# Kernel optimization log

Hardware: AMD Instinct MI355X
Metric: run time of the kernel (lower is better)

The kernel has to match this reference:

```python
import jax, jax.numpy as jnp
import numpy as np

N = 50000   # nodes
E = 600000  # directed edges
B = 128     # graphs
IN = 128
H = 128
K = 30      # sort-pool k
C_OUT = 32
KER = 5
OUT_DIM = 10
L_OUT = K - KER + 1  # 26


def setup_inputs() -> dict:
    key = jax.random.key(0)
    ks = jax.random.split(key, 12)
    s = 0.05
    return {
        "x": jax.random.normal(ks[0], (N, IN), jnp.float32),
        "edge_index": jax.random.randint(ks[1], (2, E), 0, N),
        "batch": jnp.sort(jax.random.randint(ks[2], (N,), 0, B)),
        "W0": jax.random.normal(ks[3], (IN, H), jnp.float32) * s,
        "b0": jnp.zeros((H,), jnp.float32),
        "W1": jax.random.normal(ks[4], (H, H), jnp.float32) * s,
        "b1": jnp.zeros((H,), jnp.float32),
        "W2": jax.random.normal(ks[5], (H, H), jnp.float32) * s,
        "b2": jnp.zeros((H,), jnp.float32),
        "conv_w": jax.random.normal(ks[6], (C_OUT, H, KER), jnp.float32) * s,
        "conv_b": jnp.zeros((C_OUT,), jnp.float32),
        "lin1_w": jax.random.normal(ks[7], (C_OUT * L_OUT, H), jnp.float32) * s,
        "lin1_b": jnp.zeros((H,), jnp.float32),
        "lin2_w": jax.random.normal(ks[8], (H, OUT_DIM), jnp.float32) * s,
        "lin2_b": jnp.zeros((OUT_DIM,), jnp.float32),
    }


def reference(x, edge_index, batch, W0, b0, W1, b1, W2, b2,
              conv_w, conv_b, lin1_w, lin1_b, lin2_w, lin2_b):
    # --- GCN normalization (A + I, symmetric deg^-1/2) ---
    loops = jnp.arange(N)
    row = jnp.concatenate([edge_index[0], loops])  # source
    col = jnp.concatenate([edge_index[1], loops])  # target (aggregation side)
    deg = jax.ops.segment_sum(jnp.ones_like(col, dtype=x.dtype), col, num_segments=N)
    dinv = jax.lax.rsqrt(jnp.maximum(deg, 1.0))
    norm = dinv[row] * dinv[col]  # [E+N]

    def gcn(h, W, b):
        hw = h @ W                                            # [N,H]
        msg = hw[row] * norm[:, None]                         # gather [E+N,H]
        return jax.ops.segment_sum(msg, col, num_segments=N) + b

    h = jax.nn.relu(gcn(x, W0, b0))
    h = jax.nn.relu(gcn(h, W1, b1))
    h = jax.nn.relu(gcn(h, W2, b2))

    # --- SortAggregation: per-graph sort by last channel (desc), top-K, zero-pad ---
    last = h[:, -1]
    order = jnp.lexsort((-last, batch))  # primary: batch, secondary: last desc
    hs = h[order]
    bs = batch[order]
    counts = jax.ops.segment_sum(jnp.ones((N,), jnp.int32), batch, num_segments=B)
    starts = jnp.cumsum(counts) - counts  # exclusive prefix sum
    rank = jnp.arange(N) - starts[bs]     # within-graph rank after sort
    r = jnp.where(rank < K, rank, K)      # overflow bucket K is discarded
    pooled = jnp.zeros((B, K + 1, H), h.dtype).at[bs, r].add(hs)[:, :K]  # [B,K,H]

    # --- conv1d head (NCH layout, matches torch view/transpose) ---
    xc = jnp.transpose(pooled, (0, 2, 1))  # [B,H,K]
    y = jax.lax.conv_general_dilated(xc, conv_w, (1,), "VALID",
                                     dimension_numbers=("NCH", "OIH", "NCH"))
    y = jax.nn.relu(y + conv_b[None, :, None])  # [B,C_OUT,L_OUT]
    y = y.reshape(B, -1)
    y = jax.nn.relu(y @ lin1_w + lin1_b)
    return y @ lin2_w + lin2_b  # [B,OUT_DIM]
```

## Files before the change

kernel.cpp:

```cpp
#include <hip/hip_runtime.h>
#include <math.h>

#define Nn 50000
#define Ee 600000
#define Bg 128
#define Hd 128
#define Kt 30
#define CO 32
#define KW 5
#define LOUT 26
#define CAP 2048
#define SCB 196
#define MMB 782

typedef float v2f __attribute__((ext_vector_type(2)));
typedef short bf16x8 __attribute__((ext_vector_type(8)));
typedef float f32x4 __attribute__((ext_vector_type(4)));

__device__ __forceinline__ unsigned short bfr(float v) {
    unsigned u = __builtin_bit_cast(unsigned, v);
    unsigned r = (u + 0x7FFFu + ((u >> 16) & 1u)) >> 16;
    return (unsigned short)r;
}
__device__ __forceinline__ float bff(unsigned short h) {
    unsigned u = ((unsigned)h) << 16;
    return __builtin_bit_cast(float, u);
}

__global__ void countpack_kernel(const int* __restrict__ ei, const int* __restrict__ batch,
                            int* __restrict__ deg_i, int* __restrict__ bstart,
                            const float* __restrict__ conv_w, float* __restrict__ wT2,
                            const float* __restrict__ W0, const float* __restrict__ W1,
                            const float* __restrict__ W2,
                            ushort* __restrict__ Bph, ushort* __restrict__ Bpm,
                            ushort* __restrict__ Bpl) {
    int i = blockIdx.x * 256 + threadIdx.x;
    if (i < Ee) atomicAdd(&deg_i[ei[Ee + i]], 1);
    if (i < Nn) {
        int b = batch[i];
        if (i == 0) bstart[b] = 0;
        else if (batch[i - 1] != b) bstart[b] = i;
    }
    if (i == 0) bstart[Bg] = Nn;
    if (i < CO * KW * Hd) {
        int ci = i & 127;
        int r = i >> 7;
        int o = r / KW, k = r - o * KW;
        wT2[i] = conv_w[((size_t)o * Hd + ci) * KW + k];
    }
    if (i < 3 * 2048) {
        int l = i >> 11;
        int r = i & 2047;
        int kc = r >> 9;
        int n = (r >> 6) & 7;
        int lane = r & 63;
        int m = lane & 15, kq = lane >> 4;
        const float* W = (l == 0) ? W0 : (l == 1) ? W1 : W2;
        int col = n * 16 + m;
        size_t off = ((size_t)l * 2048 + (size_t)((kc * 8 + n) * 64 + lane)) * 8;
#pragma unroll
        for (int j = 0; j < 8; ++j) {
            float v = W[(size_t)(kc * 32 + kq * 8 + j) * Hd + col];
            unsigned short h = bfr(v);
            float r1 = v - bff(h);
            unsigned short mid = bfr(r1);
            Bph[off + j] = h;
            Bpm[off + j] = mid;
            Bpl[off + j] = bfr(r1 - bff(mid));
        }
    }
}

__global__ __launch_bounds__(256) void scanBC2_kernel(const int* __restrict__ deg_i,
                            int* __restrict__ row_ptr, float* __restrict__ dinv,
                            int* __restrict__ bstart) {
    __shared__ int ls[256];
    __shared__ int boffS;
    int tid = threadIdx.x;
    int b = blockIdx.x;
    int s = 0;
    for (int k = 0; k < b; ++k)
        s += deg_i[k * 256 + tid] + 1;
    ls[tid] = s;
    __syncthreads();
    for (int off = 128; off > 0; off >>= 1) {
        if (tid < off) ls[tid] += ls[tid + off];
        __syncthreads();
    }
    if (tid == 0) boffS = ls[0];
    __syncthreads();
    int boff = boffS;
    int i = b * 256 + tid;
    int v2 = 0;
    if (i < Nn) {
        int raw = deg_i[i];
        v2 = raw + 1;
        dinv[i] = 1.0f / sqrtf((float)(raw + 2));
    }
    ls[tid] = v2;
    __syncthreads();
    for (int off = 1; off < 256; off <<= 1) {
        int t = (tid >= off) ? ls[tid - off] : 0;
        __syncthreads();
        ls[tid] += t;
        __syncthreads();
    }
    if (i < Nn) row_ptr[i + 1] = ls[tid] + boff;
    if (i == 0) row_ptr[0] = 0;
    if (b == 0 && tid == 0) {
        for (int bb = Bg - 1; bb >= 0; --bb)
            if (bstart[bb] == -1) bstart[bb] = bstart[bb + 1];
    }
}

__device__ __forceinline__ void mmx_body(int bid, int tid,
                            const float* __restrict__ Hin,
                            const ushort* __restrict__ Bph, const ushort* __restrict__ Bpm,
                            const ushort* __restrict__ Bpl,
                            const float* __restrict__ dinv, float* __restrict__ hw) {
    int w = tid >> 6, lane = tid & 63;
    int m = lane & 15, kq = lane >> 4;
    int rowA = bid * 64 + w * 16 + m;
    bool va = rowA < Nn;
    const float* ap = Hin + (size_t)rowA * Hd;
    f32x4 acc[8];
#pragma unroll
    for (int n = 0; n < 8; ++n) acc[n] = (f32x4)0.f;
#pragma unroll
    for (int kc = 0; kc < 4; ++kc) {
        bf16x8 a0 = (bf16x8)0, a1 = (bf16x8)0, a2 = (bf16x8)0;
        if (va) {
            float av[8];
            *(float4*)&av[0] = *(const float4*)(ap + kc * 32 + kq * 8);
            *(float4*)&av[4] = *(const float4*)(ap + kc * 32 + kq * 8 + 4);
#pragma unroll
            for (int j = 0; j < 8; ++j) {
                unsigned short h = bfr(av[j]);
                float r1 = av[j] - bff(h);
                unsigned short mid = bfr(r1);
                a0[j] = (short)h;
                a1[j] = (short)mid;
                a2[j] = (short)bfr(r1 - bff(mid));
            }
        }
        const ushort* bhp = Bph + (size_t)((kc * 8) * 64 + lane) * 8;
        const ushort* bmp = Bpm + (size_t)((kc * 8) * 64 + lane) * 8;
        const ushort* blp = Bpl + (size_t)((kc * 8) * 64 + lane) * 8;
#pragma unroll
        for (int n = 0; n < 8; ++n) {
            bf16x8 b0 = *(const bf16x8*)(bhp + (size_t)n * 64 * 8);
            bf16x8 b1 = *(const bf16x8*)(bmp + (size_t)n * 64 * 8);
            bf16x8 b2 = *(const bf16x8*)(blp + (size_t)n * 64 * 8);
            acc[n] = __builtin_amdgcn_mfma_f32_16x16x32_bf16(a0, b0, acc[n], 0, 0, 0);
            acc[n] = __builtin_amdgcn_mfma_f32_16x16x32_bf16(a1, b0, acc[n], 0, 0, 0);
            acc[n] = __builtin_amdgcn_mfma_f32_16x16x32_bf16(a0, b1, acc[n], 0, 0, 0);
            acc[n] = __builtin_amdgcn_mfma_f32_16x16x32_bf16(a1, b1, acc[n], 0, 0, 0);
            acc[n] = __builtin_amdgcn_mfma_f32_16x16x32_bf16(a2, b0, acc[n], 0, 0, 0);
            acc[n] = __builtin_amdgcn_mfma_f32_16x16x32_bf16(a0, b2, acc[n], 0, 0, 0);
        }
    }
    int rbase = bid * 64 + w * 16 + kq * 4;
#pragma unroll
    for (int reg = 0; reg < 4; ++reg) {
        int r = rbase + reg;
        if (r < Nn) {
            float s = dinv[r];
#pragma unroll
            for (int n = 0; n < 8; ++n)
                hw[(size_t)r * Hd + n * 16 + m] = acc[n][reg] * s;
        }
    }
}

__global__ __launch_bounds__(256) void mmx_kernel(const float* __restrict__ Hin,
                            const ushort* __restrict__ Bph, const ushort* __restrict__ Bpm,
                            const ushort* __restrict__ Bpl,
                            const float* __restrict__ dinv, float* __restrict__ hw) {
    mmx_body(blockIdx.x, threadIdx.x, Hin, Bph, Bpm, Bpl, dinv, hw);
}

__global__ __launch_bounds__(256) void mmxfill_kernel(const float* __restrict__ Hin,
                            const ushort* __restrict__ Bph, const ushort* __restrict__ Bpm,
                            const ushort* __restrict__ Bpl,
                            const float* __restrict__ dinv, float* __restrict__ hw,
                            const int* __restrict__ ei, const int* __restrict__ row_ptr,
                            int* __restrict__ cnt, int* __restrict__ csr_src) {
    if (blockIdx.x < MMB) {
        mmx_body(blockIdx.x, threadIdx.x, Hin, Bph, Bpm, Bpl, dinv, hw);
    } else {
        int e = (blockIdx.x - MMB) * 256 + threadIdx.x;
        if (e < Ee) {
            int c = ei[Ee + e];
            int r = ei[e];
            int p = row_ptr[c] + atomicAdd(&cnt[c], 1) + 1;
            csr_src[p] = r;
        }
    }
}

__global__ __launch_bounds__(256) void agg_kernel(const float* __restrict__ hw,
                            const int* __restrict__ row_ptr, const int* __restrict__ csr_src,
                            const float* __restrict__ dinv, const float* __restrict__ bias,
                            float* __restrict__ hout) {
    int node = blockIdx.x * 4 + (threadIdx.x >> 6);
    if (node >= Nn) return;
    int lane = threadIdx.x & 63;
    const v2f* hw2 = (const v2f*)hw;
    v2f a0 = hw2[(size_t)node * 64 + lane];
    v2f a1 = 0.f, a2 = 0.f, a3 = 0.f;
    int e0 = row_ptr[node], e1 = row_ptr[node + 1];
    int e = e0;
    for (; e + 3 < e1; e += 4) {
        int s0 = __builtin_nontemporal_load(csr_src + e);
        int s1 = __builtin_nontemporal_load(csr_src + e + 1);
        int s2 = __builtin_nontemporal_load(csr_src + e + 2);
        int s3 = __builtin_nontemporal_load(csr_src + e + 3);
        a0 += hw2[(size_t)s0 * 64 + lane];
        a1 += hw2[(size_t)s1 * 64 + lane];
        a2 += hw2[(size_t)s2 * 64 + lane];
        a3 += hw2[(size_t)s3 * 64 + lane];
    }
    for (; e < e1; ++e) {
        int s0 = __builtin_nontemporal_load(csr_src + e);
        a0 += hw2[(size_t)s0 * 64 + lane];
    }
    v2f acc = (a0 + a1) + (a2 + a3);
    float d = dinv[node];
    v2f bv = ((const v2f*)bias)[lane];
    v2f o;
    o.x = fmaxf(fmaf(d, acc.x, bv.x), 0.f);
    o.y = fmaxf(fmaf(d, acc.y, bv.y), 0.f);
    ((v2f*)hout)[(size_t)node * 64 + lane] = o;
}

__global__ __launch_bounds__(1024) void tail_kernel(const float* __restrict__ h,
                            const int* __restrict__ bstart,
                            const float* __restrict__ wT2, const float* __restrict__ conv_b,
                            const float* __restrict__ l1w, const float* __restrict__ l1b,
                            const float* __restrict__ l2w, const float* __restrict__ l2b,
                            float* __restrict__ out) {
    __shared__ float vals[CAP];
    __shared__ float xcl[Kt][130];
    __shared__ float fl[CO * LOUT];
    __shared__ float pz[8][Hd];
    __shared__ float z[Hd];
    __shared__ int selS[Kt];
    int b = blockIdx.x, tid = threadIdx.x;

    int s0 = bstart[b], s1 = bstart[b + 1];
    int n = s1 - s0;
    int nc = n < CAP ? n : CAP;
    if (tid < Kt) selS[tid] = -1;
    for (int j = tid; j < nc; j += 1024)
        vals[j] = h[(size_t)(s0 + j) * Hd + (Hd - 1)];
    __syncthreads();

    for (int j = tid; j < nc; j += 1024) {
        float vj = vals[j];
        int rank = 0;
        for (int i = 0; i < nc; ++i) {
            float vi = vals[i];
            rank += (vi > vj || (vi == vj && i < j)) ? 1 : 0;
        }
        if (rank < Kt) selS[rank] = s0 + j;
    }
    __syncthreads();

    for (int i = tid; i < Kt * Hd; i += 1024) {
        int t = i >> 7, c = i & 127;
        int s = selS[t];
        xcl[t][c] = (s >= 0) ? h[(size_t)s * Hd + c] : 0.f;
    }
    __syncthreads();
    if (tid < CO * LOUT) {
        int o = tid / LOUT, t = tid - o * LOUT;
        float acc = conv_b[o];
#pragma unroll
        for (int k = 0; k < KW; ++k) {
            const float* xr = &xcl[t + k][0];
            const float* wr = wT2 + ((size_t)o * KW + k) * Hd;
#pragma unroll 8
            for (int c4 = 0; c4 < 32; ++c4) {
                float2 xa = *(const float2*)(xr + c4 * 4);
                float2 xb = *(const float2*)(xr + c4 * 4 + 2);
                float4 wv = *(const float4*)(wr + c4 * 4);
                acc = fmaf(xa.x, wv.x, acc);
                acc = fmaf(xa.y, wv.y, acc);
                acc = fmaf(xb.x, wv.z, acc);
                acc = fmaf(xb.y, wv.w, acc);
            }
        }
        fl[tid] = fmaxf(acc, 0.f);
    }
    __syncthreads();
    int hh = tid & 127, chunk = tid >> 7;
    int m0 = chunk * 104;
    float acc = 0.f;
    const float* lw = l1w + (size_t)m0 * Hd + hh;
#pragma unroll 8
    for (int m = 0; m < 104; ++m)
        acc = fmaf(fl[m0 + m], lw[(size_t)m * Hd], acc);
    pz[chunk][hh] = acc;
    __syncthreads();
    if (tid < Hd) {
        float a = l1b[tid];
#pragma unroll
        for (int q = 0; q < 8; ++q) a += pz[q][tid];
        z[tid] = fmaxf(a, 0.f);
    }
    __syncthreads();
    if (tid < 10) {
        float a2 = l2b[tid];
        for (int j = 0; j < Hd; ++j)
            a2 = fmaf(z[j], l2w[j * 10 + tid], a2);
        out[b * 10 + tid] = a2;
    }
}

extern "C" void kernel_launch(void* const* d_in, const int* in_sizes, int n_in,
                              void* d_out, int out_size, void* d_ws, size_t ws_size,
                              hipStream_t stream) {
    const float* x      = (const float*)d_in[0];
    const int*   ei     = (const int*)d_in[1];
    const int*   batch  = (const int*)d_in[2];
    const float* W0     = (const float*)d_in[3];
    const float* b0     = (const float*)d_in[4];
    const float* W1     = (const float*)d_in[5];
    const float* b1     = (const float*)d_in[6];
    const float* W2     = (const float*)d_in[7];
    const float* b2     = (const float*)d_in[8];
    const float* conv_w = (const float*)d_in[9];
    const float* conv_b = (const float*)d_in[10];
    const float* l1w    = (const float*)d_in[11];
    const float* l1b    = (const float*)d_in[12];
    const float* l2w    = (const float*)d_in[13];
    const float* l2b    = (const float*)d_in[14];
    float* out = (float*)d_out;

    int* wsI = (int*)d_ws;
    size_t off = 0;
    int*   deg_i   = wsI + off; off += Nn;
    int*   cnt     = wsI + off; off += Nn;
    int*   bstart  = wsI + off; off += 132;
    int*   row_ptr = wsI + off; off += 50004;
    float* dinv    = (float*)(wsI + off); off += Nn;
    int*   csr_src = wsI + off; off += Ee;
    off = (off + 3) & ~(size_t)3;
    ushort* Bph  = (ushort*)(wsI + off); off += 3 * 16384 / 2;
    ushort* Bpm  = (ushort*)(wsI + off); off += 3 * 16384 / 2;
    ushort* Bpl  = (ushort*)(wsI + off); off += 3 * 16384 / 2;
    float* hw    = (float*)(wsI + off); off += (size_t)Nn * Hd;
    float* hbuf  = (float*)(wsI + off); off += (size_t)Nn * Hd;
    float* wT2   = (float*)(wsI + off); off += CO * KW * Hd;

    hipMemsetAsync(deg_i, 0xFF, (size_t)(Nn + Nn + 132) * 4, stream);
    countpack_kernel<<<(Ee + 255) / 256, 256, 0, stream>>>(ei, batch, deg_i, bstart,
        conv_w, wT2, W0, W1, W2, Bph, Bpm, Bpl);
    scanBC2_kernel<<<SCB, 256, 0, stream>>>(deg_i, row_ptr, dinv, bstart);
    dim3 aggGrid((Nn + 3) / 4);
    mmxfill_kernel<<<MMB + (Ee + 255) / 256, 256, 0, stream>>>(x, Bph, Bpm, Bpl,
        dinv, hw, ei, row_ptr, cnt, csr_src);
    agg_kernel<<<aggGrid, 256, 0, stream>>>(hw, row_ptr, csr_src, dinv, b0, hbuf);
    mmx_kernel<<<MMB, 256, 0, stream>>>(hbuf, Bph + 16384, Bpm + 16384, Bpl + 16384, dinv, hw);
    agg_kernel<<<aggGrid, 256, 0, stream>>>(hw, row_ptr, csr_src, dinv, b1, hbuf);
    mmx_kernel<<<MMB, 256, 0, stream>>>(hbuf, Bph + 32768, Bpm + 32768, Bpl + 32768, dinv, hw);
    agg_kernel<<<aggGrid, 256, 0, stream>>>(hw, row_ptr, csr_src, dinv, b2, hbuf);
    tail_kernel<<<Bg, 1024, 0, stream>>>(hbuf, bstart, wT2, conv_b,
                                         l1w, l1b, l2w, l2b, out);
}
```

Measured before the change: 443.7 us.

## Fuse GCN aggregation and matmul per layer via aggregate-then-transform reordering

Each GCN layer now aggregates neighbour features first (A_hat·H) into shared memory and then multiplies by W with split-bf16 MFMA in the same kernel, applying bias, ReLU and the next layer's dinv pre-scaling in the epilogue. This removes the separate hw round-trip through global memory and cuts the layer kernel launches from six to three. The CSR fill kernel is split back out as a standalone launch, so it no longer runs concurrently with the first matmul. The cost is lower occupancy from a large shared-memory tile and a serialized gather phase per block before the MFMA phase. The first layer also needs extra per-neighbour dinv loads.

```diff
diff --git a/kernel.cpp b/kernel.cpp
--- a/kernel.cpp
+++ b/kernel.cpp
@@ -11,7 +11,7 @@
 #define LOUT 26
 #define CAP 2048
 #define SCB 196
-#define MMB 782
+#define GCB 782
 
 typedef float v2f __attribute__((ext_vector_type(2)));
 typedef short bf16x8 __attribute__((ext_vector_type(8)));
@@ -113,35 +113,95 @@
     }
 }
 
-__device__ __forceinline__ void mmx_body(int bid, int tid,
-                            const float* __restrict__ Hin,
+__global__ void fill_kernel(const int* __restrict__ ei, const int* __restrict__ row_ptr,
+                            int* __restrict__ cnt, int* __restrict__ csr_src) {
+    int e = blockIdx.x * 256 + threadIdx.x;
+    if (e >= Ee) return;
+    int c = ei[Ee + e];
+    int r = ei[e];
+    int p = row_ptr[c] + atomicAdd(&cnt[c], 1) + 1;
+    csr_src[p] = r;
+}
+
+__global__ __launch_bounds__(256) void gcn_kernel(const float* __restrict__ hin,
+                            const int* __restrict__ row_ptr, const int* __restrict__ csr_src,
+                            const float* __restrict__ dinv, int scaleG,
                             const ushort* __restrict__ Bph, const ushort* __restrict__ Bpm,
                             const ushort* __restrict__ Bpl,
-                            const float* __restrict__ dinv, float* __restrict__ hw) {
-    int w = tid >> 6, lane = tid & 63;
+                            const float* __restrict__ bias, int scaleO,
+                            float* __restrict__ hout) {
+    __shared__ float gl[64][132];
+    int tid = threadIdx.x, w = tid >> 6, lane = tid & 63;
+    int nbase = blockIdx.x * 64;
+    const v2f* hin2 = (const v2f*)hin;
+
+    for (int p = 0; p < 16; ++p) {
+        int nloc = w * 16 + p;
+        int node = nbase + nloc;
+        if (node < Nn) {
+            float dn = dinv[node];
+            v2f sv = hin2[(size_t)node * 64 + lane];
+            v2f a0 = scaleG ? sv * dn : sv;
+            v2f a1 = 0.f, a2 = 0.f, a3 = 0.f;
+            int e = row_ptr[node], e1 = row_ptr[node + 1];
+            if (scaleG) {
+                for (; e + 3 < e1; e += 4) {
+                    int s0 = __builtin_nontemporal_load(csr_src + e);
+                    int s1 = __builtin_nontemporal_load(csr_src + e + 1);
+                    int s2 = __builtin_nontemporal_load(csr_src + e + 2);
+                    int s3 = __builtin_nontemporal_load(csr_src + e + 3);
+                    float d0 = dinv[s0], d1 = dinv[s1], d2 = dinv[s2], d3 = dinv[s3];
+                    a0 += hin2[(size_t)s0 * 64 + lane] * d0;
+                    a1 += hin2[(size_t)s1 * 64 + lane] * d1;
+                    a2 += hin2[(size_t)s2 * 64 + lane] * d2;
+                    a3 += hin2[(size_t)s3 * 64 + lane] * d3;
+                }
+                for (; e < e1; ++e) {
+                    int s0 = __builtin_nontemporal_load(csr_src + e);
+                    a0 += hin2[(size_t)s0 * 64 + lane] * dinv[s0];
+                }
+            } else {
+                for (; e + 3 < e1; e += 4) {
+                    int s0 = __builtin_nontemporal_load(csr_src + e);
+                    int s1 = __builtin_nontemporal_load(csr_src + e + 1);
+                    int s2 = __builtin_nontemporal_load(csr_src + e + 2);
+                    int s3 = __builtin_nontemporal_load(csr_src + e + 3);
+                    a0 += hin2[(size_t)s0 * 64 + lane];
+                    a1 += hin2[(size_t)s1 * 64 + lane];
+                    a2 += hin2[(size_t)s2 * 64 + lane];
+                    a3 += hin2[(size_t)s3 * 64 + lane];
+                }
+                for (; e < e1; ++e) {
+                    int s0 = __builtin_nontemporal_load(csr_src + e);
+                    a0 += hin2[(size_t)s0 * 64 + lane];
+                }
+            }
+            v2f g = ((a0 + a1) + (a2 + a3)) * dn;
+            gl[nloc][2 * lane] = g.x;
+            gl[nloc][2 * lane + 1] = g.y;
+        }
+    }
+    __syncthreads();
+
     int m = lane & 15, kq = lane >> 4;
-    int rowA = bid * 64 + w * 16 + m;
-    bool va = rowA < Nn;
-    const float* ap = Hin + (size_t)rowA * Hd;
     f32x4 acc[8];
 #pragma unroll
     for (int n = 0; n < 8; ++n) acc[n] = (f32x4)0.f;
+    const float* ap = &gl[w * 16 + m][0];
 #pragma unroll
     for (int kc = 0; kc < 4; ++kc) {
-        bf16x8 a0 = (bf16x8)0, a1 = (bf16x8)0, a2 = (bf16x8)0;
-        if (va) {
-            float av[8];
-            *(float4*)&av[0] = *(const float4*)(ap + kc * 32 + kq * 8);
-            *(float4*)&av[4] = *(const float4*)(ap + kc * 32 + kq * 8 + 4);
-#pragma unroll
-            for (int j = 0; j < 8; ++j) {
-                unsigned short h = bfr(av[j]);
-                float r1 = av[j] - bff(h);
-                unsigned short mid = bfr(r1);
-                a0[j] = (short)h;
-                a1[j] = (short)mid;
-                a2[j] = (short)bfr(r1 - bff(mid));
-            }
+        float av[8];
+        *(float4*)&av[0] = *(const float4*)(ap + kc * 32 + kq * 8);
+        *(float4*)&av[4] = *(const float4*)(ap + kc * 32 + kq * 8 + 4);
+        bf16x8 a0, a1, a2;
+#pragma unroll
+        for (int j = 0; j < 8; ++j) {
+            unsigned short h = bfr(av[j]);
+            float r1 = av[j] - bff(h);
+            unsigned short mid = bfr(r1);
+            a0[j] = (short)h;
+            a1[j] = (short)mid;
+            a2[j] = (short)bfr(r1 - bff(mid));
         }
         const ushort* bhp = Bph + (size_t)((kc * 8) * 64 + lane) * 8;
         const ushort* bmp = Bpm + (size_t)((kc * 8) * 64 + lane) * 8;
@@ -159,78 +219,22 @@
             acc[n] = __builtin_amdgcn_mfma_f32_16x16x32_bf16(a0, b2, acc[n], 0, 0, 0);
         }
     }
-    int rbase = bid * 64 + w * 16 + kq * 4;
+    float bv[8];
+#pragma unroll
+    for (int n = 0; n < 8; ++n) bv[n] = bias[n * 16 + m];
+    int rbase = nbase + w * 16 + kq * 4;
 #pragma unroll
     for (int reg = 0; reg < 4; ++reg) {
         int r = rbase + reg;
         if (r < Nn) {
-            float s = dinv[r];
-#pragma unroll
-            for (int n = 0; n < 8; ++n)
-                hw[(size_t)r * Hd + n * 16 + m] = acc[n][reg] * s;
-        }
-    }
-}
-
-__global__ __launch_bounds__(256) void mmx_kernel(const float* __restrict__ Hin,
-                            const ushort* __restrict__ Bph, const ushort* __restrict__ Bpm,
-                            const ushort* __restrict__ Bpl,
-                            const float* __restrict__ dinv, float* __restrict__ hw) {
-    mmx_body(blockIdx.x, threadIdx.x, Hin, Bph, Bpm, Bpl, dinv, hw);
-}
-
-__global__ __launch_bounds__(256) void mmxfill_kernel(const float* __restrict__ Hin,
-                            const ushort* __restrict__ Bph, const ushort* __restrict__ Bpm,
-                            const ushort* __restrict__ Bpl,
-                            const float* __restrict__ dinv, float* __restrict__ hw,
-                            const int* __restrict__ ei, const int* __restrict__ row_ptr,
-                            int* __restrict__ cnt, int* __restrict__ csr_src) {
-    if (blockIdx.x < MMB) {
-        mmx_body(blockIdx.x, threadIdx.x, Hin, Bph, Bpm, Bpl, dinv, hw);
-    } else {
-        int e = (blockIdx.x - MMB) * 256 + threadIdx.x;
-        if (e < Ee) {
-            int c = ei[Ee + e];
-            int r = ei[e];
-            int p = row_ptr[c] + atomicAdd(&cnt[c], 1) + 1;
-            csr_src[p] = r;
-        }
-    }
-}
-
-__global__ __launch_bounds__(256) void agg_kernel(const float* __restrict__ hw,
-                            const int* __restrict__ row_ptr, const int* __restrict__ csr_src,
-                            const float* __restrict__ dinv, const float* __restrict__ bias,
-                            float* __restrict__ hout) {
-    int node = blockIdx.x * 4 + (threadIdx.x >> 6);
-    if (node >= Nn) return;
-    int lane = threadIdx.x & 63;
-    const v2f* hw2 = (const v2f*)hw;
-    v2f a0 = hw2[(size_t)node * 64 + lane];
-    v2f a1 = 0.f, a2 = 0.f, a3 = 0.f;
-    int e0 = row_ptr[node], e1 = row_ptr[node + 1];
-    int e = e0;
-    for (; e + 3 < e1; e += 4) {
-        int s0 = __builtin_nontemporal_load(csr_src + e);
-        int s1 = __builtin_nontemporal_load(csr_src + e + 1);
-        int s2 = __builtin_nontemporal_load(csr_src + e + 2);
-        int s3 = __builtin_nontemporal_load(csr_src + e + 3);
-        a0 += hw2[(size_t)s0 * 64 + lane];
-        a1 += hw2[(size_t)s1 * 64 + lane];
-        a2 += hw2[(size_t)s2 * 64 + lane];
-        a3 += hw2[(size_t)s3 * 64 + lane];
-    }
-    for (; e < e1; ++e) {
-        int s0 = __builtin_nontemporal_load(csr_src + e);
-        a0 += hw2[(size_t)s0 * 64 + lane];
-    }
-    v2f acc = (a0 + a1) + (a2 + a3);
-    float d = dinv[node];
-    v2f bv = ((const v2f*)bias)[lane];
-    v2f o;
-    o.x = fmaxf(fmaf(d, acc.x, bv.x), 0.f);
-    o.y = fmaxf(fmaf(d, acc.y, bv.y), 0.f);
-    ((v2f*)hout)[(size_t)node * 64 + lane] = o;
+            float s = scaleO ? dinv[r] : 1.0f;
+#pragma unroll
+            for (int n = 0; n < 8; ++n) {
+                float v = fmaxf(acc[n][reg] + bv[n], 0.f) * s;
+                hout[(size_t)r * Hd + n * 16 + m] = v;
+            }
+        }
+    }
 }
 
 __global__ __launch_bounds__(1024) void tail_kernel(const float* __restrict__ h,
@@ -357,14 +361,13 @@
     countpack_kernel<<<(Ee + 255) / 256, 256, 0, stream>>>(ei, batch, deg_i, bstart,
         conv_w, wT2, W0, W1, W2, Bph, Bpm, Bpl);
     scanBC2_kernel<<<SCB, 256, 0, stream>>>(deg_i, row_ptr, dinv, bstart);
-    dim3 aggGrid((Nn + 3) / 4);
-    mmxfill_kernel<<<MMB + (Ee + 255) / 256, 256, 0, stream>>>(x, Bph, Bpm, Bpl,
-        dinv, hw, ei, row_ptr, cnt, csr_src);
-    agg_kernel<<<aggGrid, 256, 0, stream>>>(hw, row_ptr, csr_src, dinv, b0, hbuf);
-    mmx_kernel<<<MMB, 256, 0, stream>>>(hbuf, Bph + 16384, Bpm + 16384, Bpl + 16384, dinv, hw);
-    agg_kernel<<<aggGrid, 256, 0, stream>>>(hw, row_ptr, csr_src, dinv, b1, hbuf);
-    mmx_kernel<<<MMB, 256, 0, stream>>>(hbuf, Bph + 32768, Bpm + 32768, Bpl + 32768, dinv, hw);
-    agg_kernel<<<aggGrid, 256, 0, stream>>>(hw, row_ptr, csr_src, dinv, b2, hbuf);
+    fill_kernel<<<(Ee + 255) / 256, 256, 0, stream>>>(ei, row_ptr, cnt, csr_src);
+    gcn_kernel<<<GCB, 256, 0, stream>>>(x,    row_ptr, csr_src, dinv, 1,
+        Bph,         Bpm,         Bpl,         b0, 1, hbuf);
+    gcn_kernel<<<GCB, 256, 0, stream>>>(hbuf, row_ptr, csr_src, dinv, 0,
+        Bph + 16384, Bpm + 16384, Bpl + 16384, b1, 1, hw);
+    gcn_kernel<<<GCB, 256, 0, stream>>>(hw,   row_ptr, csr_src, dinv, 0,
+        Bph + 32768, Bpm + 32768, Bpl + 32768, b2, 0, hbuf);
     tail_kernel<<<Bg, 1024, 0, stream>>>(hbuf, bstart, wT2, conv_b,
                                          l1w, l1b, l2w, l2b, out);
 }
```

New measurement: 484.3 us. 1.09x slower.
